# Kernel optimization log

Measured on AMD Instinct MI355X. Metric: run time of the kernel, lower is better.

Reference implementation:

```python
import jax, jax.numpy as jnp
import numpy as np

LOC_SIZE, LOC_EMB = 100000, 256
TIM_SIZE, TIM_EMB = 48, 64
UID_SIZE, UID_EMB = 5000, 128
HID = 512
B, T = 64, 128
L_HIST, G = 1024, 4  # 256 history groups of size 4


def setup_inputs() -> dict:
    key = jax.random.key(0)
    ks = jax.random.split(key, 16)
    s = 0.02
    inp = {
        "loc": jax.random.randint(ks[0], (B, T), 0, LOC_SIZE),
        "tim": jax.random.randint(ks[1], (B, T), 0, TIM_SIZE),
        "input_lengths": jax.random.randint(ks[2], (B,), 1, T + 1),
        "history_loc": jax.random.randint(ks[3], (B, L_HIST), 0, LOC_SIZE),
        "history_tim": jax.random.randint(ks[4], (B, L_HIST), 0, TIM_SIZE),
        "history_uid": jax.random.randint(ks[5], (B, L_HIST), 0, UID_SIZE),
        "group_size": G,
        "emb_loc": jax.random.normal(ks[6], (LOC_SIZE, LOC_EMB), jnp.float32) * s,
        "emb_tim": jax.random.normal(ks[7], (TIM_SIZE, TIM_EMB), jnp.float32) * s,
        "emb_uid": jax.random.normal(ks[8], (UID_SIZE, UID_EMB), jnp.float32) * s,
        "W_attn": jax.random.normal(ks[9], (HID, LOC_EMB + TIM_EMB + UID_EMB), jnp.float32) * s,
        "b_attn": jnp.zeros((HID,), jnp.float32),
        "W_ih": jax.random.normal(ks[10], (3 * HID, LOC_EMB + TIM_EMB), jnp.float32) * s,
        "b_ih": jnp.zeros((3 * HID,), jnp.float32),
        "W_hh": jax.random.normal(ks[11], (3 * HID, HID), jnp.float32) * s,
        "b_hh": jnp.zeros((3 * HID,), jnp.float32),
        "W_final": jax.random.normal(ks[12], (UID_SIZE, 3 * HID), jnp.float32) * s,
        "b_final": jnp.zeros((UID_SIZE,), jnp.float32),
    }
    return inp


def _gru(x_seq, W_ih, b_ih, W_hh, b_hh):
    # x_seq: [T, B, Din] -> outputs [T, B, H], PyTorch gate order (r, z, n)
    H = W_hh.shape[1]
    gx = jnp.einsum("tbd,gd->tbg", x_seq, W_ih) + b_ih  # [T,B,3H]
    h0 = jnp.zeros((x_seq.shape[1], H), x_seq.dtype)

    def step(h, gx_t):
        gh = h @ W_hh.T + b_hh
        xr, xz, xn = jnp.split(gx_t, 3, axis=-1)
        hr, hz, hn = jnp.split(gh, 3, axis=-1)
        r = jax.nn.sigmoid(xr + hr)
        z = jax.nn.sigmoid(xz + hz)
        n = jnp.tanh(xn + r * hn)
        h_new = (1.0 - z) * n + z * h
        return h_new, h_new

    _, outs = jax.lax.scan(step, h0, gx)
    return outs  # [T,B,H]


def reference(loc, tim, input_lengths, history_loc, history_tim, history_uid,
              group_size, emb_loc, emb_tim, emb_uid, W_attn, b_attn,
              W_ih, b_ih, W_hh, b_hh, W_final, b_final):
    Bn, Tn = loc.shape
    # current-trajectory embeddings -> GRU (dropout is identity in eval)
    x = jnp.concatenate([emb_loc[loc], emb_tim[tim]], axis=-1)  # [B,T,Din]
    outs = _gru(jnp.swapaxes(x, 0, 1), W_ih, b_ih, W_hh, b_hh)  # [T,B,H]
    outs = jnp.swapaxes(outs, 0, 1)                              # [B,T,H]
    last = outs[jnp.arange(Bn), input_lengths - 1]               # [B,H]

    # history pooling: groups of size G; uid emb averaged within group,
    # loc/tim embeddings taken at each group's first element
    Gc = group_size
    n_groups = history_uid.shape[1] // Gc
    uid_h = emb_uid[history_uid].reshape(Bn, n_groups, Gc, -1).mean(axis=2)  # [B,N,Du]
    loc_h = emb_loc[history_loc[:, ::Gc]]                                    # [B,N,Dl]
    tim_h = emb_tim[history_tim[:, ::Gc]]                                    # [B,N,Dt]
    hist = jnp.concatenate([loc_h, tim_h, uid_h], axis=-1)
    hist = jnp.tanh(jnp.einsum("bnd,hd->bnh", hist, W_attn) + b_attn)        # [B,N,H]

    # 'dot' attention: replaces the nested python-loop scoring
    energies = jnp.einsum("bh,bnh->bn", last, hist)
    attn_w = jax.nn.softmax(energies, axis=-1)
    context = jnp.einsum("bn,bnh->bh", attn_w, hist)

    out = jnp.concatenate([last, context, last], axis=-1)  # [B,3H]
    y = out @ W_final.T + b_final                          # [B,U]
    # original assigns y (one row) into score[t] of shape [T,U] -> broadcast over T
    score = jnp.broadcast_to(y[:, None, :], (Bn, Tn, y.shape[-1]))
    return score
```

## Files before the change

kernel.cpp:

```cpp
#include <hip/hip_runtime.h>
#include <hip/hip_bf16.h>


typedef __attribute__((ext_vector_type(8))) short bf16x8;
typedef __attribute__((ext_vector_type(4))) float f32x4;
typedef __attribute__((ext_vector_type(4))) unsigned short u16x4;
typedef __attribute__((ext_vector_type(2))) unsigned long long u64x2;
typedef unsigned long long u64;

__device__ inline unsigned short f2bf(float x) {
  __hip_bfloat16 b = __float2bfloat16(x);
  return __builtin_bit_cast(unsigned short, b);
}

__global__ void gather_x(const int* __restrict__ loc, const int* __restrict__ tim,
                         const float* __restrict__ eloc, const float* __restrict__ etim,
                         float* __restrict__ X) {
  int row = blockIdx.x;
  int t = row >> 6, b = row & 63;
  int tid = threadIdx.x;
  float4* dst = (float4*)(X + (size_t)row * 320);
  int li = loc[b * 128 + t];
  dst[tid] = ((const float4*)(eloc + (size_t)li * 256))[tid];
  if (tid < 16) {
    int ti = tim[b * 128 + t];
    dst[64 + tid] = ((const float4*)(etim + (size_t)ti * 64))[tid];
  }
}

__global__ void hist_feat(const int* __restrict__ hloc, const int* __restrict__ htim,
                          const int* __restrict__ huid,
                          const float* __restrict__ eloc, const float* __restrict__ etim,
                          const float* __restrict__ euid, float* __restrict__ histf) {
  int row = blockIdx.x;
  int b = row >> 8, n = row & 255;
  int tid = threadIdx.x;
  int base = b * 1024 + (n << 2);
  float4* dst = (float4*)(histf + (size_t)row * 448);
  {
    int li = hloc[base];
    dst[tid] = ((const float4*)(eloc + (size_t)li * 256))[tid];
  }
  if (tid < 16) {
    int ti = htim[base];
    dst[64 + tid] = ((const float4*)(etim + (size_t)ti * 64))[tid];
  }
  if (tid < 32) {
    const float4* u0 = (const float4*)(euid + (size_t)huid[base + 0] * 128);
    const float4* u1 = (const float4*)(euid + (size_t)huid[base + 1] * 128);
    const float4* u2 = (const float4*)(euid + (size_t)huid[base + 2] * 128);
    const float4* u3 = (const float4*)(euid + (size_t)huid[base + 3] * 128);
    float4 v0 = u0[tid], v1 = u1[tid], v2 = u2[tid], v3 = u3[tid];
    float4 o;
    o.x = 0.25f * (v0.x + v1.x + v2.x + v3.x);
    o.y = 0.25f * (v0.y + v1.y + v2.y + v3.y);
    o.z = 0.25f * (v0.z + v1.z + v2.z + v3.z);
    o.w = 0.25f * (v0.w + v1.w + v2.w + v3.w);
    dst[80 + tid] = o;
  }
}

template<bool TANH>
__global__ __launch_bounds__(256)
void gemm_bf16(const float* __restrict__ A, const float* __restrict__ Bm,
               const float* __restrict__ bias, float* __restrict__ C,
               int M, int N, int K) {
  constexpr int LDR = 40;
  __shared__ short Asl[128 * LDR];
  __shared__ short Bsl[128 * LDR];
  const int tid = threadIdx.x;
  const int lane = tid & 63, wid = tid >> 6;
  const int wr = wid >> 1, wc = wid & 1;
  const int m16 = lane & 15, g4 = lane >> 4;
  const int bm = blockIdx.y * 128, bn = blockIdx.x * 128;
  const int srow = tid >> 1, shalf = tid & 1;
  f32x4 acc[4][4] = {};
  for (int k0 = 0; k0 < K; k0 += 32) {
    {
      const float* ap = A + (size_t)(bm + srow) * K + k0 + (shalf << 4);
      float4 f0 = ((const float4*)ap)[0], f1 = ((const float4*)ap)[1];
      float4 f2 = ((const float4*)ap)[2], f3 = ((const float4*)ap)[3];
      bf16x8 w0, w1;
      w0[0]=(short)f2bf(f0.x); w0[1]=(short)f2bf(f0.y); w0[2]=(short)f2bf(f0.z); w0[3]=(short)f2bf(f0.w);
      w0[4]=(short)f2bf(f1.x); w0[5]=(short)f2bf(f1.y); w0[6]=(short)f2bf(f1.z); w0[7]=(short)f2bf(f1.w);
      w1[0]=(short)f2bf(f2.x); w1[1]=(short)f2bf(f2.y); w1[2]=(short)f2bf(f2.z); w1[3]=(short)f2bf(f2.w);
      w1[4]=(short)f2bf(f3.x); w1[5]=(short)f2bf(f3.y); w1[6]=(short)f2bf(f3.z); w1[7]=(short)f2bf(f3.w);
      short* arow = Asl + srow * LDR + (shalf << 4);
      *(bf16x8*)(arow)     = w0;
      *(bf16x8*)(arow + 8) = w1;
      const float* bp = Bm + (size_t)(bn + srow) * K + k0 + (shalf << 4);
      f0 = ((const float4*)bp)[0]; f1 = ((const float4*)bp)[1];
      f2 = ((const float4*)bp)[2]; f3 = ((const float4*)bp)[3];
      w0[0]=(short)f2bf(f0.x); w0[1]=(short)f2bf(f0.y); w0[2]=(short)f2bf(f0.z); w0[3]=(short)f2bf(f0.w);
      w0[4]=(short)f2bf(f1.x); w0[5]=(short)f2bf(f1.y); w0[6]=(short)f2bf(f1.z); w0[7]=(short)f2bf(f1.w);
      w1[0]=(short)f2bf(f2.x); w1[1]=(short)f2bf(f2.y); w1[2]=(short)f2bf(f2.z); w1[3]=(short)f2bf(f2.w);
      w1[4]=(short)f2bf(f3.x); w1[5]=(short)f2bf(f3.y); w1[6]=(short)f2bf(f3.z); w1[7]=(short)f2bf(f3.w);
      short* brow = Bsl + srow * LDR + (shalf << 4);
      *(bf16x8*)(brow)     = w0;
      *(bf16x8*)(brow + 8) = w1;
    }
    __syncthreads();
    bf16x8 af[4], bfr[4];
#pragma unroll
    for (int i = 0; i < 4; ++i) {
      int ra = (wr << 6) + (i << 4) + m16;
      af[i]  = *(const bf16x8*)(Asl + ra * LDR + (g4 << 3));
      int rb = (wc << 6) + (i << 4) + m16;
      bfr[i] = *(const bf16x8*)(Bsl + rb * LDR + (g4 << 3));
    }
#pragma unroll
    for (int i = 0; i < 4; ++i)
#pragma unroll
      for (int j = 0; j < 4; ++j)
        acc[i][j] = __builtin_amdgcn_mfma_f32_16x16x32_bf16(af[i], bfr[j], acc[i][j], 0, 0, 0);
    __syncthreads();
  }
#pragma unroll
  for (int i = 0; i < 4; ++i) {
#pragma unroll
    for (int j = 0; j < 4; ++j) {
      int col = bn + (wc << 6) + (j << 4) + m16;
      float bv = bias[col];
#pragma unroll
      for (int q = 0; q < 4; ++q) {
        int row = bm + (wr << 6) + (i << 4) + (g4 << 2) + q;
        float v = acc[i][j][q] + bv;
        if (TANH) v = tanhf(v);
        C[(size_t)row * N + col] = v;
      }
    }
  }
}

__global__ __launch_bounds__(128)
void gru_persist(const float* __restrict__ gx, const float* __restrict__ W_hh,
                 const float* __restrict__ b_hh, const int* __restrict__ lens,
                 short* __restrict__ h_bf, float* __restrict__ lastb,
                 unsigned int* __restrict__ flags) {
  __shared__ short wlds[6 * 16 * 512];
  const int tid = threadIdx.x;
  const int lane = tid & 63, tt = tid >> 6;
  const int bid = blockIdx.x;
  const int c = bid >> 2, grp = bid & 3;
  const int j0 = (c << 5) + (tt << 4);
  const int b0 = grp << 4;
  const int m16 = lane & 15, g4 = lane >> 4;

  for (int gi = 0; gi < 3; ++gi) {
    const float* wg = W_hh + (size_t)(gi * 512 + j0) * 512;
    short* slab = wlds + (((gi << 1) + tt) << 13);
    for (int r = 0; r < 16; ++r) {
      int k = lane << 3;
      const float4* src = (const float4*)(wg + (size_t)r * 512 + k);
      float4 f0 = src[0], f1 = src[1];
      bf16x8 w;
      w[0]=(short)f2bf(f0.x); w[1]=(short)f2bf(f0.y); w[2]=(short)f2bf(f0.z); w[3]=(short)f2bf(f0.w);
      w[4]=(short)f2bf(f1.x); w[5]=(short)f2bf(f1.y); w[6]=(short)f2bf(f1.z); w[7]=(short)f2bf(f1.w);
      int off = ((r << 9) + k) ^ ((r & 7) << 3);
      *(bf16x8*)(slab + off) = w;
    }
  }
  __syncthreads();

  const int bcol = b0 + m16;
  const int jr = j0 + (g4 << 2);
  const f32x4 bhr = *(const f32x4*)&b_hh[jr];
  const f32x4 bhz = *(const f32x4*)&b_hh[512 + jr];
  const f32x4 bhn = *(const f32x4*)&b_hh[1024 + jr];
  const int lenb = lens[bcol];
  f32x4 hprev = {0.f, 0.f, 0.f, 0.f};

  unsigned int* gflags = flags + (grp << 8);
  unsigned int* ownflag = gflags + (c << 4);

  for (int t = 0; t < 128; ++t) {
    const float* gxb = gx + ((size_t)t * 64 + bcol) * 1536;
    f32x4 gr = *(const f32x4*)(gxb + jr);
    f32x4 gz = *(const f32x4*)(gxb + 512 + jr);
    f32x4 gn = *(const f32x4*)(gxb + 1024 + jr);
    f32x4 ar = {0.f, 0.f, 0.f, 0.f}, az = ar, an = ar;
    if (t) {
      unsigned tgt = (unsigned)t;
      while (true) {
        unsigned f = tgt;
        if (lane < 16)
          f = __hip_atomic_load(gflags + (lane << 4), __ATOMIC_RELAXED, __HIP_MEMORY_SCOPE_AGENT);
        if (__all((int)(f >= tgt))) break;
      }
      asm volatile("" ::: "memory");

      const u64* hp = (const u64*)(h_bf + ((t & 1) << 15) + (size_t)bcol * 512 + (g4 << 3));
      u64 hu[32];
#pragma unroll
      for (int ks = 0; ks < 16; ++ks) {
        hu[2 * ks]     = __hip_atomic_load(hp + ks * 8,     __ATOMIC_RELAXED, __HIP_MEMORY_SCOPE_AGENT);
        hu[2 * ks + 1] = __hip_atomic_load(hp + ks * 8 + 1, __ATOMIC_RELAXED, __HIP_MEMORY_SCOPE_AGENT);
      }
#define GRU_MFMA(ks)                                                                 \
      {                                                                              \
        u64x2 p; p[0] = hu[2 * (ks)]; p[1] = hu[2 * (ks) + 1];                       \
        bf16x8 hf = __builtin_bit_cast(bf16x8, p);                                   \
        int off = ((m16 << 9) + ((ks) << 5) + (g4 << 3)) ^ ((m16 & 7) << 3);         \
        ar = __builtin_amdgcn_mfma_f32_16x16x32_bf16(*(const bf16x8*)(wlds + ((0 + tt) << 13) + off), hf, ar, 0, 0, 0); \
        az = __builtin_amdgcn_mfma_f32_16x16x32_bf16(*(const bf16x8*)(wlds + ((2 + tt) << 13) + off), hf, az, 0, 0, 0); \
        an = __builtin_amdgcn_mfma_f32_16x16x32_bf16(*(const bf16x8*)(wlds + ((4 + tt) << 13) + off), hf, an, 0, 0, 0); \
      }
      GRU_MFMA(0)  GRU_MFMA(1)  GRU_MFMA(2)  GRU_MFMA(3)
      GRU_MFMA(4)  GRU_MFMA(5)  GRU_MFMA(6)  GRU_MFMA(7)
      GRU_MFMA(8)  GRU_MFMA(9)  GRU_MFMA(10) GRU_MFMA(11)
      GRU_MFMA(12) GRU_MFMA(13) GRU_MFMA(14) GRU_MFMA(15)
#undef GRU_MFMA
    }
    u16x4 hw;
#pragma unroll
    for (int q = 0; q < 4; ++q) {
      float r = 1.f / (1.f + __expf(-(gr[q] + ar[q] + bhr[q])));
      float z = 1.f / (1.f + __expf(-(gz[q] + az[q] + bhz[q])));
      float xn = gn[q] + r * (an[q] + bhn[q]);
      float n = 1.f - 2.f / (__expf(2.f * xn) + 1.f);
      float hv = (1.f - z) * n + z * hprev[q];
      hprev[q] = hv;
      hw[q] = f2bf(hv);
    }
    __hip_atomic_store((u64*)(h_bf + ((~t & 1) << 15) + (size_t)bcol * 512 + jr),
                       __builtin_bit_cast(u64, hw),
                       __ATOMIC_RELAXED, __HIP_MEMORY_SCOPE_AGENT);
    if (t == lenb - 1) {
      *(f32x4*)(lastb + (size_t)bcol * 512 + jr) = hprev;
    }
    if (t < 127) {
      asm volatile("s_waitcnt vmcnt(0)" ::: "memory");
      __syncthreads();
      if (tid == 0)
        __hip_atomic_store(ownflag, (unsigned)(t + 1), __ATOMIC_RELAXED, __HIP_MEMORY_SCOPE_AGENT);
    }
  }
}

__global__ __launch_bounds__(256)
void attn_ctx(const float* __restrict__ histt, const float* __restrict__ last,
              float* __restrict__ ctx) {
  int b = blockIdx.x, tid = threadIdx.x;
  __shared__ float ls[512];
  __shared__ float w[256];
  __shared__ float red[256];
  ((float2*)ls)[tid] = ((const float2*)(last + (size_t)b * 512))[tid];
  __syncthreads();
  const float* hb = histt + (size_t)b * 256 * 512;
  const float* hrow = hb + (size_t)tid * 512;
  float acc = 0.f;
  for (int k = 0; k < 512; k += 4) {
    float4 h4 = *(const float4*)(hrow + k);
    acc += ls[k] * h4.x + ls[k + 1] * h4.y + ls[k + 2] * h4.z + ls[k + 3] * h4.w;
  }
  red[tid] = acc;
  __syncthreads();
  for (int s = 128; s; s >>= 1) {
    if (tid < s) red[tid] = fmaxf(red[tid], red[tid + s]);
    __syncthreads();
  }
  float m = red[0];
  __syncthreads();
  float ex = expf(acc - m);
  w[tid] = ex; red[tid] = ex;
  __syncthreads();
  for (int s = 128; s; s >>= 1) {
    if (tid < s) red[tid] += red[tid + s];
    __syncthreads();
  }
  float inv = 1.f / red[0];
  float c0 = 0.f, c1 = 0.f;
  for (int n = 0; n < 256; ++n) {
    float wn = w[n];
    c0 += wn * hb[(size_t)n * 512 + tid];
    c1 += wn * hb[(size_t)n * 512 + tid + 256];
  }
  ctx[(size_t)b * 512 + tid]       = c0 * inv;
  ctx[(size_t)b * 512 + tid + 256] = c1 * inv;
}

__global__ __launch_bounds__(256)
void final_gemm(const float* __restrict__ last, const float* __restrict__ ctx,
                const float* __restrict__ Wf, const float* __restrict__ bf,
                float* __restrict__ y) {
  __shared__ float s[64][129];
  const int tid = threadIdx.x;
  const int u0 = blockIdx.x << 3;
  const int ul = tid >> 6, b = tid & 63;
  float acc0 = 0.f, acc1 = 0.f;
  for (int kc = 0; kc < 12; ++kc) {
    __syncthreads();
    for (int i = tid; i < 2048; i += 256) {
      int rb = i >> 5, cc = (i & 31) << 2;
      int k = kc * 128 + cc;
      const float* src = (k < 512) ? (last + (size_t)rb * 512 + k)
                       : (k < 1024) ? (ctx + (size_t)rb * 512 + k - 512)
                                    : (last + (size_t)rb * 512 + k - 1024);
      float4 v = *(const float4*)src;
      s[rb][cc] = v.x; s[rb][cc + 1] = v.y; s[rb][cc + 2] = v.z; s[rb][cc + 3] = v.w;
    }
    __syncthreads();
#pragma unroll
    for (int uu = 0; uu < 2; ++uu) {
      int u = u0 + ul + uu * 4;
      const float* wrow = Wf + (size_t)u * 1536 + kc * 128;
      float a = 0.f;
#pragma unroll 8
      for (int c = 0; c < 128; c += 4) {
        float4 w4 = *(const float4*)(wrow + c);
        a += w4.x * s[b][c] + w4.y * s[b][c + 1] + w4.z * s[b][c + 2] + w4.w * s[b][c + 3];
      }
      if (uu == 0) acc0 += a; else acc1 += a;
    }
  }
  int u = u0 + ul;
  y[(size_t)b * 5000 + u]     = acc0 + bf[u];
  y[(size_t)b * 5000 + u + 4] = acc1 + bf[u + 4];
}

__global__ void broadcast_y(const float* __restrict__ y, float* __restrict__ out) {
  int bt = blockIdx.x;
  const float4* src = (const float4*)(y + (size_t)(bt >> 7) * 5000);
  float4* dst = (float4*)(out + (size_t)bt * 5000);
  for (int i = threadIdx.x; i < 1250; i += 256) dst[i] = src[i];
}

extern "C" void kernel_launch(void* const* d_in, const int* in_sizes, int n_in,
                              void* d_out, int out_size, void* d_ws, size_t ws_size,
                              hipStream_t stream) {
  const int* loc  = (const int*)d_in[0];
  const int* tim  = (const int*)d_in[1];
  const int* lens = (const int*)d_in[2];
  const int* hloc = (const int*)d_in[3];
  const int* htim = (const int*)d_in[4];
  const int* huid = (const int*)d_in[5];
  const float* eloc    = (const float*)d_in[7];
  const float* etim    = (const float*)d_in[8];
  const float* euid    = (const float*)d_in[9];
  const float* W_attn  = (const float*)d_in[10];
  const float* b_attn  = (const float*)d_in[11];
  const float* W_ih    = (const float*)d_in[12];
  const float* b_ih    = (const float*)d_in[13];
  const float* W_hh    = (const float*)d_in[14];
  const float* b_hh    = (const float*)d_in[15];
  const float* W_final = (const float*)d_in[16];
  const float* b_final = (const float*)d_in[17];
  float* out = (float*)d_out;
  char* ws = (char*)d_ws;

  float* X     = (float*)(ws + 0ull);
  float* gx    = (float*)(ws + 10485760ull);
  float* histf = (float*)(ws + 60817408ull);
  float* histt = (float*)(ws + 90177536ull);
  float* lastb = (float*)(ws + 123731968ull);
  float* ctx   = (float*)(ws + 123863040ull);
  float* yv    = (float*)(ws + 123994112ull);
  short* h_bf  = (short*)(ws + 125274112ull);
  unsigned int* flags = (unsigned int*)(ws + 60817408ull);

  gather_x<<<8192, 64, 0, stream>>>(loc, tim, eloc, etim, X);
  gemm_bf16<false><<<dim3(12, 64), 256, 0, stream>>>(X, W_ih, b_ih, gx, 8192, 1536, 320);
  hist_feat<<<16384, 64, 0, stream>>>(hloc, htim, huid, eloc, etim, euid, histf);
  gemm_bf16<true><<<dim3(4, 128), 256, 0, stream>>>(histf, W_attn, b_attn, histt, 16384, 512, 448);

  hipMemsetAsync(flags, 0, 4096, stream);
  gru_persist<<<64, 128, 0, stream>>>(gx, W_hh, b_hh, lens, h_bf, lastb, flags);

  attn_ctx<<<64, 256, 0, stream>>>(histt, lastb, ctx);
  final_gemm<<<625, 256, 0, stream>>>(lastb, ctx, W_final, b_final, yv);
  broadcast_y<<<8192, 256, 0, stream>>>(yv, out);
}
```

Baseline: 692.5 us.

## Fuse embedding gathers, input/attention GEMMs and GRU into one persistent overlapped kernel

Merges the embedding gathers into the A-tile loads of the two GEMMs, which removes the X and histf intermediate buffers. Places the gx GEMM, the history-attention GEMM and the GRU recurrence in a single launch with role-partitioned blocks. GRU blocks poll per-row-tile counters so each timestep can start as soon as its gx rows are written, overlapping the serial recurrence with the GEMM work. This trades extra launch and memory traffic for spin-wait synchronisation and fewer blocks per GEMM, and correctness depends on all 172 blocks being co-resident.

```diff
diff --git a/kernel.cpp b/kernel.cpp
--- a/kernel.cpp
+++ b/kernel.cpp
@@ -8,156 +8,175 @@
 typedef __attribute__((ext_vector_type(2))) unsigned long long u64x2;
 typedef unsigned long long u64;
 
+#define GXB 96
+#define ATB 44
+#define GRUB 32
+
 __device__ inline unsigned short f2bf(float x) {
   __hip_bfloat16 b = __float2bfloat16(x);
   return __builtin_bit_cast(unsigned short, b);
 }
-
-__global__ void gather_x(const int* __restrict__ loc, const int* __restrict__ tim,
-                         const float* __restrict__ eloc, const float* __restrict__ etim,
-                         float* __restrict__ X) {
-  int row = blockIdx.x;
-  int t = row >> 6, b = row & 63;
-  int tid = threadIdx.x;
-  float4* dst = (float4*)(X + (size_t)row * 320);
-  int li = loc[b * 128 + t];
-  dst[tid] = ((const float4*)(eloc + (size_t)li * 256))[tid];
-  if (tid < 16) {
-    int ti = tim[b * 128 + t];
-    dst[64 + tid] = ((const float4*)(etim + (size_t)ti * 64))[tid];
-  }
-}
-
-__global__ void hist_feat(const int* __restrict__ hloc, const int* __restrict__ htim,
-                          const int* __restrict__ huid,
-                          const float* __restrict__ eloc, const float* __restrict__ etim,
-                          const float* __restrict__ euid, float* __restrict__ histf) {
-  int row = blockIdx.x;
-  int b = row >> 8, n = row & 255;
-  int tid = threadIdx.x;
-  int base = b * 1024 + (n << 2);
-  float4* dst = (float4*)(histf + (size_t)row * 448);
-  {
-    int li = hloc[base];
-    dst[tid] = ((const float4*)(eloc + (size_t)li * 256))[tid];
-  }
-  if (tid < 16) {
-    int ti = htim[base];
-    dst[64 + tid] = ((const float4*)(etim + (size_t)ti * 64))[tid];
-  }
-  if (tid < 32) {
-    const float4* u0 = (const float4*)(euid + (size_t)huid[base + 0] * 128);
-    const float4* u1 = (const float4*)(euid + (size_t)huid[base + 1] * 128);
-    const float4* u2 = (const float4*)(euid + (size_t)huid[base + 2] * 128);
-    const float4* u3 = (const float4*)(euid + (size_t)huid[base + 3] * 128);
-    float4 v0 = u0[tid], v1 = u1[tid], v2 = u2[tid], v3 = u3[tid];
-    float4 o;
-    o.x = 0.25f * (v0.x + v1.x + v2.x + v3.x);
-    o.y = 0.25f * (v0.y + v1.y + v2.y + v3.y);
-    o.z = 0.25f * (v0.z + v1.z + v2.z + v3.z);
-    o.w = 0.25f * (v0.w + v1.w + v2.w + v3.w);
-    dst[80 + tid] = o;
-  }
-}
-
-template<bool TANH>
+__device__ inline bf16x8 pack8(float4 a, float4 b) {
+  bf16x8 w;
+  w[0]=(short)f2bf(a.x); w[1]=(short)f2bf(a.y); w[2]=(short)f2bf(a.z); w[3]=(short)f2bf(a.w);
+  w[4]=(short)f2bf(b.x); w[5]=(short)f2bf(b.y); w[6]=(short)f2bf(b.z); w[7]=(short)f2bf(b.w);
+  return w;
+}
+
 __global__ __launch_bounds__(256)
-void gemm_bf16(const float* __restrict__ A, const float* __restrict__ Bm,
-               const float* __restrict__ bias, float* __restrict__ C,
-               int M, int N, int K) {
-  constexpr int LDR = 40;
-  __shared__ short Asl[128 * LDR];
-  __shared__ short Bsl[128 * LDR];
+void phase1(const int* __restrict__ loc, const int* __restrict__ tim,
+            const int* __restrict__ lens,
+            const int* __restrict__ hloc, const int* __restrict__ htim,
+            const int* __restrict__ huid,
+            const float* __restrict__ eloc, const float* __restrict__ etim,
+            const float* __restrict__ euid,
+            const float* __restrict__ W_attn, const float* __restrict__ b_attn,
+            const float* __restrict__ W_ih, const float* __restrict__ b_ih,
+            const float* __restrict__ W_hh, const float* __restrict__ b_hh,
+            float* __restrict__ gx, float* __restrict__ histt,
+            short* __restrict__ h_bf, float* __restrict__ lastb,
+            unsigned int* __restrict__ sync) {
+  __shared__ short smem[6 * 16 * 512];
+  const int bid = blockIdx.x;
   const int tid = threadIdx.x;
-  const int lane = tid & 63, wid = tid >> 6;
-  const int wr = wid >> 1, wc = wid & 1;
-  const int m16 = lane & 15, g4 = lane >> 4;
-  const int bm = blockIdx.y * 128, bn = blockIdx.x * 128;
-  const int srow = tid >> 1, shalf = tid & 1;
-  f32x4 acc[4][4] = {};
-  for (int k0 = 0; k0 < K; k0 += 32) {
-    {
-      const float* ap = A + (size_t)(bm + srow) * K + k0 + (shalf << 4);
-      float4 f0 = ((const float4*)ap)[0], f1 = ((const float4*)ap)[1];
-      float4 f2 = ((const float4*)ap)[2], f3 = ((const float4*)ap)[3];
-      bf16x8 w0, w1;
-      w0[0]=(short)f2bf(f0.x); w0[1]=(short)f2bf(f0.y); w0[2]=(short)f2bf(f0.z); w0[3]=(short)f2bf(f0.w);
-      w0[4]=(short)f2bf(f1.x); w0[5]=(short)f2bf(f1.y); w0[6]=(short)f2bf(f1.z); w0[7]=(short)f2bf(f1.w);
-      w1[0]=(short)f2bf(f2.x); w1[1]=(short)f2bf(f2.y); w1[2]=(short)f2bf(f2.z); w1[3]=(short)f2bf(f2.w);
-      w1[4]=(short)f2bf(f3.x); w1[5]=(short)f2bf(f3.y); w1[6]=(short)f2bf(f3.z); w1[7]=(short)f2bf(f3.w);
-      short* arow = Asl + srow * LDR + (shalf << 4);
-      *(bf16x8*)(arow)     = w0;
-      *(bf16x8*)(arow + 8) = w1;
-      const float* bp = Bm + (size_t)(bn + srow) * K + k0 + (shalf << 4);
-      f0 = ((const float4*)bp)[0]; f1 = ((const float4*)bp)[1];
-      f2 = ((const float4*)bp)[2]; f3 = ((const float4*)bp)[3];
-      w0[0]=(short)f2bf(f0.x); w0[1]=(short)f2bf(f0.y); w0[2]=(short)f2bf(f0.z); w0[3]=(short)f2bf(f0.w);
-      w0[4]=(short)f2bf(f1.x); w0[5]=(short)f2bf(f1.y); w0[6]=(short)f2bf(f1.z); w0[7]=(short)f2bf(f1.w);
-      w1[0]=(short)f2bf(f2.x); w1[1]=(short)f2bf(f2.y); w1[2]=(short)f2bf(f2.z); w1[3]=(short)f2bf(f2.w);
-      w1[4]=(short)f2bf(f3.x); w1[5]=(short)f2bf(f3.y); w1[6]=(short)f2bf(f3.z); w1[7]=(short)f2bf(f3.w);
-      short* brow = Bsl + srow * LDR + (shalf << 4);
-      *(bf16x8*)(brow)     = w0;
-      *(bf16x8*)(brow + 8) = w1;
-    }
-    __syncthreads();
-    bf16x8 af[4], bfr[4];
-#pragma unroll
-    for (int i = 0; i < 4; ++i) {
-      int ra = (wr << 6) + (i << 4) + m16;
-      af[i]  = *(const bf16x8*)(Asl + ra * LDR + (g4 << 3));
-      int rb = (wc << 6) + (i << 4) + m16;
-      bfr[i] = *(const bf16x8*)(Bsl + rb * LDR + (g4 << 3));
-    }
-#pragma unroll
-    for (int i = 0; i < 4; ++i)
-#pragma unroll
-      for (int j = 0; j < 4; ++j)
-        acc[i][j] = __builtin_amdgcn_mfma_f32_16x16x32_bf16(af[i], bfr[j], acc[i][j], 0, 0, 0);
-    __syncthreads();
-  }
-#pragma unroll
-  for (int i = 0; i < 4; ++i) {
-#pragma unroll
-    for (int j = 0; j < 4; ++j) {
-      int col = bn + (wc << 6) + (j << 4) + m16;
-      float bv = bias[col];
-#pragma unroll
-      for (int q = 0; q < 4; ++q) {
-        int row = bm + (wr << 6) + (i << 4) + (g4 << 2) + q;
-        float v = acc[i][j][q] + bv;
-        if (TANH) v = tanhf(v);
-        C[(size_t)row * N + col] = v;
-      }
-    }
-  }
-}
-
-__global__ __launch_bounds__(128)
-void gru_persist(const float* __restrict__ gx, const float* __restrict__ W_hh,
-                 const float* __restrict__ b_hh, const int* __restrict__ lens,
-                 short* __restrict__ h_bf, float* __restrict__ lastb,
-                 unsigned int* __restrict__ flags) {
-  __shared__ short wlds[6 * 16 * 512];
-  const int tid = threadIdx.x;
-  const int lane = tid & 63, tt = tid >> 6;
-  const int bid = blockIdx.x;
-  const int c = bid >> 2, grp = bid & 3;
+
+  if (bid < GXB + ATB) {
+    constexpr int LDR = 40;
+    short* Asl = smem;
+    short* Bsl = smem + 128 * LDR;
+    const int lane = tid & 63, wid = tid >> 6;
+    const int wr = wid >> 1, wc = wid & 1;
+    const int m16 = lane & 15, g4 = lane >> 4;
+    const int srow = tid >> 1, shalf = tid & 1;
+    const bool isgx = bid < GXB;
+    const int ntiles = isgx ? 768 : 512;
+    const int stride = isgx ? GXB : ATB;
+    const int NT     = isgx ? 12 : 4;
+    const int Kdim   = isgx ? 320 : 448;
+    const int Ndim   = isgx ? 1536 : 512;
+    const float* Bmat = isgx ? W_ih : W_attn;
+    const float* bias = isgx ? b_ih : b_attn;
+    for (int tile = isgx ? bid : (bid - GXB); tile < ntiles; tile += stride) {
+      const int yt = tile / NT, nt = tile % NT;
+      const int bm = yt << 7, bn = nt << 7;
+      f32x4 acc[4][4] = {};
+      for (int k0 = 0; k0 < Kdim; k0 += 32) {
+        {
+          const int grow = bm + srow;
+          float4 f0, f1, f2, f3;
+          if (isgx) {
+            const int t = grow >> 6, b = grow & 63;
+            const float* ap = (k0 < 256)
+              ? eloc + (size_t)loc[b * 128 + t] * 256 + k0 + (shalf << 4)
+              : etim + (size_t)tim[b * 128 + t] * 64 + (k0 - 256) + (shalf << 4);
+            f0 = ((const float4*)ap)[0]; f1 = ((const float4*)ap)[1];
+            f2 = ((const float4*)ap)[2]; f3 = ((const float4*)ap)[3];
+          } else {
+            const int b = grow >> 8, n = grow & 255;
+            const int base = b * 1024 + (n << 2);
+            if (k0 < 256) {
+              const float* ap = eloc + (size_t)hloc[base] * 256 + k0 + (shalf << 4);
+              f0 = ((const float4*)ap)[0]; f1 = ((const float4*)ap)[1];
+              f2 = ((const float4*)ap)[2]; f3 = ((const float4*)ap)[3];
+            } else if (k0 < 320) {
+              const float* ap = etim + (size_t)htim[base] * 64 + (k0 - 256) + (shalf << 4);
+              f0 = ((const float4*)ap)[0]; f1 = ((const float4*)ap)[1];
+              f2 = ((const float4*)ap)[2]; f3 = ((const float4*)ap)[3];
+            } else {
+              const int cu = (k0 - 320) + (shalf << 4);
+              const float4* u0 = (const float4*)(euid + (size_t)huid[base + 0] * 128 + cu);
+              const float4* u1 = (const float4*)(euid + (size_t)huid[base + 1] * 128 + cu);
+              const float4* u2 = (const float4*)(euid + (size_t)huid[base + 2] * 128 + cu);
+              const float4* u3 = (const float4*)(euid + (size_t)huid[base + 3] * 128 + cu);
+#define AVG4(idx, dst) { float4 a=u0[idx],b4=u1[idx],c4=u2[idx],d4=u3[idx];            \
+        dst.x=0.25f*(a.x+b4.x+c4.x+d4.x); dst.y=0.25f*(a.y+b4.y+c4.y+d4.y);           \
+        dst.z=0.25f*(a.z+b4.z+c4.z+d4.z); dst.w=0.25f*(a.w+b4.w+c4.w+d4.w); }
+              AVG4(0, f0) AVG4(1, f1) AVG4(2, f2) AVG4(3, f3)
+#undef AVG4
+            }
+          }
+          short* arow = Asl + srow * LDR + (shalf << 4);
+          *(bf16x8*)(arow)     = pack8(f0, f1);
+          *(bf16x8*)(arow + 8) = pack8(f2, f3);
+        }
+        {
+          const float* bp = Bmat + (size_t)(bn + srow) * Kdim + k0 + (shalf << 4);
+          float4 f0 = ((const float4*)bp)[0], f1 = ((const float4*)bp)[1];
+          float4 f2 = ((const float4*)bp)[2], f3 = ((const float4*)bp)[3];
+          short* brow = Bsl + srow * LDR + (shalf << 4);
+          *(bf16x8*)(brow)     = pack8(f0, f1);
+          *(bf16x8*)(brow + 8) = pack8(f2, f3);
+        }
+        __syncthreads();
+        bf16x8 af[4], bfr[4];
+#pragma unroll
+        for (int i = 0; i < 4; ++i) {
+          af[i]  = *(const bf16x8*)(Asl + ((wr << 6) + (i << 4) + m16) * LDR + (g4 << 3));
+          bfr[i] = *(const bf16x8*)(Bsl + ((wc << 6) + (i << 4) + m16) * LDR + (g4 << 3));
+        }
+#pragma unroll
+        for (int i = 0; i < 4; ++i)
+#pragma unroll
+          for (int j = 0; j < 4; ++j)
+            acc[i][j] = __builtin_amdgcn_mfma_f32_16x16x32_bf16(af[i], bfr[j], acc[i][j], 0, 0, 0);
+        __syncthreads();
+      }
+      if (isgx) {
+#pragma unroll
+        for (int i = 0; i < 4; ++i)
+#pragma unroll
+          for (int j = 0; j < 4; ++j) {
+            const int col = bn + (wc << 6) + (j << 4) + m16;
+            const float bv = bias[col];
+#pragma unroll
+            for (int q = 0; q < 4; ++q) {
+              const int row = bm + (wr << 6) + (i << 4) + (g4 << 2) + q;
+              gx[(size_t)row * 1536 + col] = acc[i][j][q] + bv;
+            }
+          }
+        asm volatile("s_waitcnt vmcnt(0)" ::: "memory");
+        __syncthreads();
+        if (tid == 0) {
+          __hip_atomic_fetch_add(sync + 512 + yt, 1u, __ATOMIC_RELEASE, __HIP_MEMORY_SCOPE_AGENT);
+          asm volatile("s_waitcnt vmcnt(0)" ::: "memory");
+          __hip_atomic_fetch_add(sync + 576, 1u, __ATOMIC_RELAXED, __HIP_MEMORY_SCOPE_AGENT);
+        }
+      } else {
+#pragma unroll
+        for (int i = 0; i < 4; ++i)
+#pragma unroll
+          for (int j = 0; j < 4; ++j) {
+            const int col = bn + (wc << 6) + (j << 4) + m16;
+            const float bv = bias[col];
+#pragma unroll
+            for (int q = 0; q < 4; ++q) {
+              const int row = bm + (wr << 6) + (i << 4) + (g4 << 2) + q;
+              histt[(size_t)row * 512 + col] = tanhf(acc[i][j][q] + bv);
+            }
+          }
+      }
+    }
+    return;
+  }
+
+  const int bid2 = bid - (GXB + ATB);
+  const int w = tid >> 6, lane = tid & 63;
+  const int gp = bid2 & 1, c = bid2 >> 1;
+  const int grp = (gp << 1) | (w >> 1), tt = w & 1;
   const int j0 = (c << 5) + (tt << 4);
   const int b0 = grp << 4;
   const int m16 = lane & 15, g4 = lane >> 4;
 
-  for (int gi = 0; gi < 3; ++gi) {
-    const float* wg = W_hh + (size_t)(gi * 512 + j0) * 512;
-    short* slab = wlds + (((gi << 1) + tt) << 13);
-    for (int r = 0; r < 16; ++r) {
-      int k = lane << 3;
-      const float4* src = (const float4*)(wg + (size_t)r * 512 + k);
-      float4 f0 = src[0], f1 = src[1];
-      bf16x8 w;
-      w[0]=(short)f2bf(f0.x); w[1]=(short)f2bf(f0.y); w[2]=(short)f2bf(f0.z); w[3]=(short)f2bf(f0.w);
-      w[4]=(short)f2bf(f1.x); w[5]=(short)f2bf(f1.y); w[6]=(short)f2bf(f1.z); w[7]=(short)f2bf(f1.w);
-      int off = ((r << 9) + k) ^ ((r & 7) << 3);
-      *(bf16x8*)(slab + off) = w;
+  if (w < 2) {
+    for (int gi = 0; gi < 3; ++gi) {
+      const float* wg = W_hh + (size_t)(gi * 512 + j0) * 512;
+      short* slab = smem + (((gi << 1) + tt) << 13);
+      for (int r = 0; r < 16; ++r) {
+        const int k = lane << 3;
+        const float4* src = (const float4*)(wg + (size_t)r * 512 + k);
+        const int off = ((r << 9) + k) ^ ((r & 7) << 3);
+        *(bf16x8*)(slab + off) = pack8(src[0], src[1]);
+      }
     }
   }
   __syncthreads();
@@ -170,17 +189,41 @@
   const int lenb = lens[bcol];
   f32x4 hprev = {0.f, 0.f, 0.f, 0.f};
 
-  unsigned int* gflags = flags + (grp << 8);
+  unsigned int* gflags = sync + (gp << 8);
   unsigned int* ownflag = gflags + (c << 4);
+  bool all_done = false;
 
   for (int t = 0; t < 128; ++t) {
-    const float* gxb = gx + ((size_t)t * 64 + bcol) * 1536;
-    f32x4 gr = *(const f32x4*)(gxb + jr);
-    f32x4 gz = *(const f32x4*)(gxb + 512 + jr);
-    f32x4 gn = *(const f32x4*)(gxb + 1024 + jr);
+    if (!all_done) {
+      if (__hip_atomic_load(sync + 576, __ATOMIC_RELAXED, __HIP_MEMORY_SCOPE_AGENT) == 768u)
+        all_done = true;
+      else {
+        const int yt = t >> 1;
+        while (__hip_atomic_load(sync + 512 + yt, __ATOMIC_RELAXED, __HIP_MEMORY_SCOPE_AGENT) < 12u) {
+          if (__hip_atomic_load(sync + 576, __ATOMIC_RELAXED, __HIP_MEMORY_SCOPE_AGENT) == 768u) {
+            all_done = true; break;
+          }
+        }
+      }
+      asm volatile("" ::: "memory");
+    }
+    const u64* gxp = (const u64*)(gx + ((size_t)t * 64 + bcol) * 1536 + jr);
+    u64 g0 = __hip_atomic_load(gxp,       __ATOMIC_RELAXED, __HIP_MEMORY_SCOPE_AGENT);
+    u64 g1 = __hip_atomic_load(gxp + 1,   __ATOMIC_RELAXED, __HIP_MEMORY_SCOPE_AGENT);
+    u64 g2 = __hip_atomic_load(gxp + 256, __ATOMIC_RELAXED, __HIP_MEMORY_SCOPE_AGENT);
+    u64 g3 = __hip_atomic_load(gxp + 257, __ATOMIC_RELAXED, __HIP_MEMORY_SCOPE_AGENT);
+    u64 g4v= __hip_atomic_load(gxp + 512, __ATOMIC_RELAXED, __HIP_MEMORY_SCOPE_AGENT);
+    u64 g5 = __hip_atomic_load(gxp + 513, __ATOMIC_RELAXED, __HIP_MEMORY_SCOPE_AGENT);
+    u64x2 p0; p0[0] = g0; p0[1] = g1;
+    u64x2 p1; p1[0] = g2; p1[1] = g3;
+    u64x2 p2; p2[0] = g4v; p2[1] = g5;
+    f32x4 gr = __builtin_bit_cast(f32x4, p0);
+    f32x4 gz = __builtin_bit_cast(f32x4, p1);
+    f32x4 gn = __builtin_bit_cast(f32x4, p2);
+
     f32x4 ar = {0.f, 0.f, 0.f, 0.f}, az = ar, an = ar;
     if (t) {
-      unsigned tgt = (unsigned)t;
+      const unsigned tgt = (unsigned)t;
       while (true) {
         unsigned f = tgt;
         if (lane < 16)
@@ -201,9 +244,9 @@
         u64x2 p; p[0] = hu[2 * (ks)]; p[1] = hu[2 * (ks) + 1];                       \
         bf16x8 hf = __builtin_bit_cast(bf16x8, p);                                   \
         int off = ((m16 << 9) + ((ks) << 5) + (g4 << 3)) ^ ((m16 & 7) << 3);         \
-        ar = __builtin_amdgcn_mfma_f32_16x16x32_bf16(*(const bf16x8*)(wlds + ((0 + tt) << 13) + off), hf, ar, 0, 0, 0); \
-        az = __builtin_amdgcn_mfma_f32_16x16x32_bf16(*(const bf16x8*)(wlds + ((2 + tt) << 13) + off), hf, az, 0, 0, 0); \
-        an = __builtin_amdgcn_mfma_f32_16x16x32_bf16(*(const bf16x8*)(wlds + ((4 + tt) << 13) + off), hf, an, 0, 0, 0); \
+        ar = __builtin_amdgcn_mfma_f32_16x16x32_bf16(*(const bf16x8*)(smem + ((0 + tt) << 13) + off), hf, ar, 0, 0, 0); \
+        az = __builtin_amdgcn_mfma_f32_16x16x32_bf16(*(const bf16x8*)(smem + ((2 + tt) << 13) + off), hf, az, 0, 0, 0); \
+        an = __builtin_amdgcn_mfma_f32_16x16x32_bf16(*(const bf16x8*)(smem + ((4 + tt) << 13) + off), hf, an, 0, 0, 0); \
       }
       GRU_MFMA(0)  GRU_MFMA(1)  GRU_MFMA(2)  GRU_MFMA(3)
       GRU_MFMA(4)  GRU_MFMA(5)  GRU_MFMA(6)  GRU_MFMA(7)
@@ -348,23 +391,19 @@
   float* out = (float*)d_out;
   char* ws = (char*)d_ws;
 
-  float* X     = (float*)(ws + 0ull);
-  float* gx    = (float*)(ws + 10485760ull);
-  float* histf = (float*)(ws + 60817408ull);
-  float* histt = (float*)(ws + 90177536ull);
-  float* lastb = (float*)(ws + 123731968ull);
-  float* ctx   = (float*)(ws + 123863040ull);
-  float* yv    = (float*)(ws + 123994112ull);
-  short* h_bf  = (short*)(ws + 125274112ull);
-  unsigned int* flags = (unsigned int*)(ws + 60817408ull);
-
-  gather_x<<<8192, 64, 0, stream>>>(loc, tim, eloc, etim, X);
-  gemm_bf16<false><<<dim3(12, 64), 256, 0, stream>>>(X, W_ih, b_ih, gx, 8192, 1536, 320);
-  hist_feat<<<16384, 64, 0, stream>>>(hloc, htim, huid, eloc, etim, euid, histf);
-  gemm_bf16<true><<<dim3(4, 128), 256, 0, stream>>>(histf, W_attn, b_attn, histt, 16384, 512, 448);
-
-  hipMemsetAsync(flags, 0, 4096, stream);
-  gru_persist<<<64, 128, 0, stream>>>(gx, W_hh, b_hh, lens, h_bf, lastb, flags);
+  float* gx    = (float*)(ws + 0ull);
+  float* histt = (float*)(ws + 50331648ull);
+  float* lastb = (float*)(ws + 83886080ull);
+  float* ctx   = (float*)(ws + 84017152ull);
+  float* yv    = (float*)(ws + 84148224ull);
+  short* h_bf  = (short*)(ws + 85428224ull);
+  unsigned int* sync = (unsigned int*)(ws + 85559296ull);
+
+  hipMemsetAsync(sync, 0, 4096, stream);
+  phase1<<<GXB + ATB + GRUB, 256, 0, stream>>>(
+      loc, tim, lens, hloc, htim, huid, eloc, etim, euid,
+      W_attn, b_attn, W_ih, b_ih, W_hh, b_hh,
+      gx, histt, h_bf, lastb, sync);
 
   attn_ctx<<<64, 256, 0, stream>>>(histt, lastb, ctx);
   final_gemm<<<625, 256, 0, stream>>>(lastb, ctx, W_final, b_final, yv);
```

Result: slower. 940.7 us (+35.8%).

## Replace GRU flag barrier with sentinel-polled per-step hidden buffers

Applied to the files above, without the earlier changes.

The persistent GRU kernel no longer publishes and polls per-block step flags with a block barrier and a vmcnt wait each step. Instead it writes every step's hidden state to its own slot in a buffer pre-filled with 0xFFFF, and consumers poll the h words directly until no sentinel remains. Each batch group also stops at the longest sequence length among its 16 rows, and the two embedding gather kernels are merged into one launch. The trade-off is an extra 8 MB memset, the assumption that 0xFFFF never appears as a real bf16 value, and removal of a __syncthreads after the LDS weight load, which relies on each wave reading only the slab it wrote itself.

```diff
diff --git a/kernel.cpp b/kernel.cpp
--- a/kernel.cpp
+++ b/kernel.cpp
@@ -13,50 +13,48 @@
   return __builtin_bit_cast(unsigned short, b);
 }
 
-__global__ void gather_x(const int* __restrict__ loc, const int* __restrict__ tim,
-                         const float* __restrict__ eloc, const float* __restrict__ etim,
-                         float* __restrict__ X) {
-  int row = blockIdx.x;
-  int t = row >> 6, b = row & 63;
-  int tid = threadIdx.x;
-  float4* dst = (float4*)(X + (size_t)row * 320);
-  int li = loc[b * 128 + t];
-  dst[tid] = ((const float4*)(eloc + (size_t)li * 256))[tid];
-  if (tid < 16) {
-    int ti = tim[b * 128 + t];
-    dst[64 + tid] = ((const float4*)(etim + (size_t)ti * 64))[tid];
-  }
-}
-
-__global__ void hist_feat(const int* __restrict__ hloc, const int* __restrict__ htim,
-                          const int* __restrict__ huid,
-                          const float* __restrict__ eloc, const float* __restrict__ etim,
-                          const float* __restrict__ euid, float* __restrict__ histf) {
-  int row = blockIdx.x;
-  int b = row >> 8, n = row & 255;
-  int tid = threadIdx.x;
-  int base = b * 1024 + (n << 2);
-  float4* dst = (float4*)(histf + (size_t)row * 448);
-  {
-    int li = hloc[base];
+__global__ void prep(const int* __restrict__ loc, const int* __restrict__ tim,
+                     const int* __restrict__ hloc, const int* __restrict__ htim,
+                     const int* __restrict__ huid,
+                     const float* __restrict__ eloc, const float* __restrict__ etim,
+                     const float* __restrict__ euid,
+                     float* __restrict__ X, float* __restrict__ histf) {
+  int bid = blockIdx.x, tid = threadIdx.x;
+  if (bid < 8192) {
+    int t = bid >> 6, b = bid & 63;
+    float4* dst = (float4*)(X + (size_t)bid * 320);
+    int li = loc[b * 128 + t];
     dst[tid] = ((const float4*)(eloc + (size_t)li * 256))[tid];
-  }
-  if (tid < 16) {
-    int ti = htim[base];
-    dst[64 + tid] = ((const float4*)(etim + (size_t)ti * 64))[tid];
-  }
-  if (tid < 32) {
-    const float4* u0 = (const float4*)(euid + (size_t)huid[base + 0] * 128);
-    const float4* u1 = (const float4*)(euid + (size_t)huid[base + 1] * 128);
-    const float4* u2 = (const float4*)(euid + (size_t)huid[base + 2] * 128);
-    const float4* u3 = (const float4*)(euid + (size_t)huid[base + 3] * 128);
-    float4 v0 = u0[tid], v1 = u1[tid], v2 = u2[tid], v3 = u3[tid];
-    float4 o;
-    o.x = 0.25f * (v0.x + v1.x + v2.x + v3.x);
-    o.y = 0.25f * (v0.y + v1.y + v2.y + v3.y);
-    o.z = 0.25f * (v0.z + v1.z + v2.z + v3.z);
-    o.w = 0.25f * (v0.w + v1.w + v2.w + v3.w);
-    dst[80 + tid] = o;
+    if (tid < 16) {
+      int ti = tim[b * 128 + t];
+      dst[64 + tid] = ((const float4*)(etim + (size_t)ti * 64))[tid];
+    }
+  } else {
+    int row = bid - 8192;
+    int b = row >> 8, n = row & 255;
+    int base = b * 1024 + (n << 2);
+    float4* dst = (float4*)(histf + (size_t)row * 448);
+    {
+      int li = hloc[base];
+      dst[tid] = ((const float4*)(eloc + (size_t)li * 256))[tid];
+    }
+    if (tid < 16) {
+      int ti = htim[base];
+      dst[64 + tid] = ((const float4*)(etim + (size_t)ti * 64))[tid];
+    }
+    if (tid < 32) {
+      const float4* u0 = (const float4*)(euid + (size_t)huid[base + 0] * 128);
+      const float4* u1 = (const float4*)(euid + (size_t)huid[base + 1] * 128);
+      const float4* u2 = (const float4*)(euid + (size_t)huid[base + 2] * 128);
+      const float4* u3 = (const float4*)(euid + (size_t)huid[base + 3] * 128);
+      float4 v0 = u0[tid], v1 = u1[tid], v2 = u2[tid], v3 = u3[tid];
+      float4 o;
+      o.x = 0.25f * (v0.x + v1.x + v2.x + v3.x);
+      o.y = 0.25f * (v0.y + v1.y + v2.y + v3.y);
+      o.z = 0.25f * (v0.z + v1.z + v2.z + v3.z);
+      o.w = 0.25f * (v0.w + v1.w + v2.w + v3.w);
+      dst[80 + tid] = o;
+    }
   }
 }
 
@@ -103,10 +101,8 @@
     bf16x8 af[4], bfr[4];
 #pragma unroll
     for (int i = 0; i < 4; ++i) {
-      int ra = (wr << 6) + (i << 4) + m16;
-      af[i]  = *(const bf16x8*)(Asl + ra * LDR + (g4 << 3));
-      int rb = (wc << 6) + (i << 4) + m16;
-      bfr[i] = *(const bf16x8*)(Bsl + rb * LDR + (g4 << 3));
+      af[i]  = *(const bf16x8*)(Asl + ((wr << 6) + (i << 4) + m16) * LDR + (g4 << 3));
+      bfr[i] = *(const bf16x8*)(Bsl + ((wc << 6) + (i << 4) + m16) * LDR + (g4 << 3));
     }
 #pragma unroll
     for (int i = 0; i < 4; ++i)
@@ -135,8 +131,7 @@
 __global__ __launch_bounds__(128)
 void gru_persist(const float* __restrict__ gx, const float* __restrict__ W_hh,
                  const float* __restrict__ b_hh, const int* __restrict__ lens,
-                 short* __restrict__ h_bf, float* __restrict__ lastb,
-                 unsigned int* __restrict__ flags) {
+                 short* __restrict__ h_all, float* __restrict__ lastb) {
   __shared__ short wlds[6 * 16 * 512];
   const int tid = threadIdx.x;
   const int lane = tid & 63, tt = tid >> 6;
@@ -160,7 +155,6 @@
       *(bf16x8*)(slab + off) = w;
     }
   }
-  __syncthreads();
 
   const int bcol = b0 + m16;
   const int jr = j0 + (g4 << 2);
@@ -168,33 +162,32 @@
   const f32x4 bhz = *(const f32x4*)&b_hh[512 + jr];
   const f32x4 bhn = *(const f32x4*)&b_hh[1024 + jr];
   const int lenb = lens[bcol];
+  int tmax = 0;
+  for (int i = 0; i < 16; ++i) tmax = max(tmax, lens[b0 + i]);
   f32x4 hprev = {0.f, 0.f, 0.f, 0.f};
 
-  unsigned int* gflags = flags + (grp << 8);
-  unsigned int* ownflag = gflags + (c << 4);
-
-  for (int t = 0; t < 128; ++t) {
+  for (int t = 0; t < tmax; ++t) {
     const float* gxb = gx + ((size_t)t * 64 + bcol) * 1536;
     f32x4 gr = *(const f32x4*)(gxb + jr);
     f32x4 gz = *(const f32x4*)(gxb + 512 + jr);
     f32x4 gn = *(const f32x4*)(gxb + 1024 + jr);
     f32x4 ar = {0.f, 0.f, 0.f, 0.f}, az = ar, an = ar;
     if (t) {
-      unsigned tgt = (unsigned)t;
-      while (true) {
-        unsigned f = tgt;
-        if (lane < 16)
-          f = __hip_atomic_load(gflags + (lane << 4), __ATOMIC_RELAXED, __HIP_MEMORY_SCOPE_AGENT);
-        if (__all((int)(f >= tgt))) break;
-      }
-      asm volatile("" ::: "memory");
-
-      const u64* hp = (const u64*)(h_bf + ((t & 1) << 15) + (size_t)bcol * 512 + (g4 << 3));
+      const u64* hp = (const u64*)(h_all + (size_t)(t - 1) * 32768 + (size_t)bcol * 512 + (g4 << 3));
       u64 hu[32];
-#pragma unroll
-      for (int ks = 0; ks < 16; ++ks) {
-        hu[2 * ks]     = __hip_atomic_load(hp + ks * 8,     __ATOMIC_RELAXED, __HIP_MEMORY_SCOPE_AGENT);
-        hu[2 * ks + 1] = __hip_atomic_load(hp + ks * 8 + 1, __ATOMIC_RELAXED, __HIP_MEMORY_SCOPE_AGENT);
+      unsigned miss = 0xFFFFFFFFu;
+      while (miss) {
+        unsigned nm = 0;
+#pragma unroll
+        for (int k2 = 0; k2 < 32; ++k2) {
+          if (miss & (1u << k2))
+            hu[k2] = __hip_atomic_load(hp + ((k2 >> 1) << 3) + (k2 & 1),
+                                       __ATOMIC_RELAXED, __HIP_MEMORY_SCOPE_AGENT);
+        }
+#pragma unroll
+        for (int k2 = 0; k2 < 32; ++k2)
+          if ((unsigned short)(hu[k2] & 0xFFFFu) == 0xFFFFu) nm |= (1u << k2);
+        miss = nm;
       }
 #define GRU_MFMA(ks)                                                                 \
       {                                                                              \
@@ -222,17 +215,11 @@
       hprev[q] = hv;
       hw[q] = f2bf(hv);
     }
-    __hip_atomic_store((u64*)(h_bf + ((~t & 1) << 15) + (size_t)bcol * 512 + jr),
+    __hip_atomic_store((u64*)(h_all + (size_t)t * 32768 + (size_t)bcol * 512 + jr),
                        __builtin_bit_cast(u64, hw),
                        __ATOMIC_RELAXED, __HIP_MEMORY_SCOPE_AGENT);
     if (t == lenb - 1) {
       *(f32x4*)(lastb + (size_t)bcol * 512 + jr) = hprev;
-    }
-    if (t < 127) {
-      asm volatile("s_waitcnt vmcnt(0)" ::: "memory");
-      __syncthreads();
-      if (tid == 0)
-        __hip_atomic_store(ownflag, (unsigned)(t + 1), __ATOMIC_RELAXED, __HIP_MEMORY_SCOPE_AGENT);
     }
   }
 }
@@ -348,23 +335,21 @@
   float* out = (float*)d_out;
   char* ws = (char*)d_ws;
 
-  float* X     = (float*)(ws + 0ull);
-  float* gx    = (float*)(ws + 10485760ull);
+  float* gx    = (float*)(ws + 0ull);
+  float* X     = (float*)(ws + 50331648ull);
   float* histf = (float*)(ws + 60817408ull);
+  short* h_all = (short*)(ws + 60817408ull);
   float* histt = (float*)(ws + 90177536ull);
   float* lastb = (float*)(ws + 123731968ull);
   float* ctx   = (float*)(ws + 123863040ull);
   float* yv    = (float*)(ws + 123994112ull);
-  short* h_bf  = (short*)(ws + 125274112ull);
-  unsigned int* flags = (unsigned int*)(ws + 60817408ull);
-
-  gather_x<<<8192, 64, 0, stream>>>(loc, tim, eloc, etim, X);
+
+  prep<<<24576, 64, 0, stream>>>(loc, tim, hloc, htim, huid, eloc, etim, euid, X, histf);
   gemm_bf16<false><<<dim3(12, 64), 256, 0, stream>>>(X, W_ih, b_ih, gx, 8192, 1536, 320);
-  hist_feat<<<16384, 64, 0, stream>>>(hloc, htim, huid, eloc, etim, euid, histf);
   gemm_bf16<true><<<dim3(4, 128), 256, 0, stream>>>(histf, W_attn, b_attn, histt, 16384, 512, 448);
 
-  hipMemsetAsync(flags, 0, 4096, stream);
-  gru_persist<<<64, 128, 0, stream>>>(gx, W_hh, b_hh, lens, h_bf, lastb, flags);
+  hipMemsetAsync(h_all, 0xFF, 128 * 64 * 512 * sizeof(short), stream);
+  gru_persist<<<64, 128, 0, stream>>>(gx, W_hh, b_hh, lens, h_all, lastb);
 
   attn_ctx<<<64, 256, 0, stream>>>(histt, lastb, ctx);
   final_gemm<<<625, 256, 0, stream>>>(lastb, ctx, W_final, b_final, yv);
```

After: 851.5 us. +23.0%, slower.
